# Performance work log

Measured on AMD Instinct MI355X. Metric: run time of the kernel, lower is better.

Reference implementation:

```python
import math
import jax, jax.numpy as jnp
import numpy as np

N_BASIS = 512   # number of basis signals (linear input dim)
FRAME_LEN = 64  # L, basis signal length (linear output dim)
BATCH = 8
FRAMES = 16000


def overlap_and_add(signal, frame_step):
    """Faithful jax port of the torch overlap_and_add (subframe index_add).

    signal: (..., frames, frame_length)
    returns: (..., frame_step*(frames-1)+frame_length)
    """
    *outer, frames, frame_length = signal.shape
    sub_len = math.gcd(frame_length, frame_step)
    sub_step = frame_step // sub_len
    spf = frame_length // sub_len               # subframes per frame
    output_size = frame_step * (frames - 1) + frame_length
    out_sub = output_size // sub_len

    # (..., frames*spf, sub_len)
    subframe_signal = signal.reshape(*outer, frames * spf, sub_len)

    # static scatter indices, same as torch.arange(out_sub).unfold(0, spf, sub_step)
    idx = (np.arange(frames)[:, None] * sub_step + np.arange(spf)[None, :]).reshape(-1)
    idx = jnp.asarray(idx, dtype=jnp.int32)

    result = jnp.zeros((*outer, out_sub, sub_len), dtype=signal.dtype)
    result = result.at[..., idx, :].add(subframe_signal)
    return result.reshape(*outer, out_sub * sub_len)


def setup_inputs() -> dict:
    key = jax.random.key(0)
    k1, k2 = jax.random.split(key)
    weight = jax.random.normal(k1, (BATCH, FRAMES, N_BASIS), dtype=jnp.float32)
    basis_signal_weight = jax.random.normal(k2, (FRAME_LEN, N_BASIS), dtype=jnp.float32)
    return {"weight": weight, "basis_signal_weight": basis_signal_weight}


def reference(weight, basis_signal_weight):
    L = FRAME_LEN
    # nn.Linear with bias=False: source = weight @ W.T ; W: (L, N)
    source = jnp.einsum("bkn,ln->bkl", weight, basis_signal_weight)  # (B, K, L)
    return overlap_and_add(source, L // 2)
```

## Files before the change

### kernel.cpp

```cpp
#include <hip/hip_runtime.h>
#include <hip/hip_bf16.h>

typedef __bf16 bf16x8 __attribute__((ext_vector_type(8)));
typedef __bf16 bf16x4 __attribute__((ext_vector_type(4)));
typedef float  f32x4  __attribute__((ext_vector_type(4)));

#define N_BASIS   512
#define FRAME_LEN 64
#define BATCH     8
#define FRAMES    16000
#define STEP      32
#define OUT_PER_BATCH (STEP * (FRAMES - 1) + FRAME_LEN)

#define WAVES            8
#define BLOCK            (WAVES * 64)
#define FPB              (WAVES * 16)
#define TPBATCH          (FRAMES / FPB)
#define TOTAL_TILES      (BATCH * TPBATCH)
#define TILES_PER_BLOCK  2
#define GRID             (TOTAL_TILES / TILES_PER_BLOCK)

__global__ __launch_bounds__(BLOCK, 4)
void basis_ola_kernel(const float* __restrict__ weight,
                      const float* __restrict__ basis,
                      float* __restrict__ out)
{
    __shared__ __bf16 Wlds[FRAME_LEN * N_BASIS];
    __shared__ float xbuf[2][WAVES][2][16];

    const int tid = threadIdx.x;

    for (int q = tid; q < (FRAME_LEN * N_BASIS) / 4; q += BLOCK) {
        const int e = q * 4;
        const int c = e >> 9;
        const float4 v = *(const float4*)(basis + e);
        bf16x4 b;
        b[0] = (__bf16)v.x; b[1] = (__bf16)v.y;
        b[2] = (__bf16)v.z; b[3] = (__bf16)v.w;
        *(bf16x4*)(&Wlds[e ^ ((c & 7) << 3)]) = b;
    }
    __syncthreads();

    const int wave = tid >> 6;
    const int lane = tid & 63;
    const int lo   = lane & 15;
    const int hi   = lane >> 4;

    const int g0 = blockIdx.x * TILES_PER_BLOCK;

    if (wave == 0) {
        const int bb0 = g0 / TPBATCH, t0 = g0 % TPBATCH;
        float val = 0.f;
        if (t0 > 0) {
            const int c  = 32 + (lane >> 1);
            const int kh = (lane & 1) * 256;
            const float* wr = weight + ((size_t)bb0 * FRAMES + (size_t)t0 * FPB - 1) * N_BASIS;
            for (int n = kh; n < kh + 256; n += 8) {
                const float4 a0 = *(const float4*)(wr + n);
                const float4 a1 = *(const float4*)(wr + n + 4);
                const int e = ((c << 9) + n) ^ ((c & 7) << 3);
                const bf16x8 bw = *(const bf16x8*)(&Wlds[e]);
                val += a0.x*(float)bw[0] + a0.y*(float)bw[1] + a0.z*(float)bw[2] + a0.w*(float)bw[3]
                     + a1.x*(float)bw[4] + a1.y*(float)bw[5] + a1.z*(float)bw[6] + a1.w*(float)bw[7];
            }
        }
        val += __shfl_xor(val, 1);
        if ((lane & 1) == 0) {
            const int cc = lane >> 1;
            xbuf[1][WAVES - 1][cc >> 4][cc & 15] = val;
        }
    }

    for (int ti = 0; ti < TILES_PER_BLOCK; ++ti) {
        const int g    = g0 + ti;
        const int bb   = g / TPBATCH;
        const int tile = g % TPBATCH;
        const int F0   = tile * FPB;
        const int p    = ti & 1;

        const float* arow = weight +
            ((size_t)bb * FRAMES + F0 + wave * 16 + lo) * (size_t)N_BASIS;

        f32x4 acc[4] = {};

        #pragma unroll 2
        for (int ks = 0; ks < N_BASIS / 32; ++ks) {
            const int kk = ks * 32;
            const float4 a0 = *(const float4*)(arow + kk + hi * 8);
            const float4 a1 = *(const float4*)(arow + kk + hi * 8 + 4);
            bf16x8 af;
            af[0] = (__bf16)a0.x; af[1] = (__bf16)a0.y;
            af[2] = (__bf16)a0.z; af[3] = (__bf16)a0.w;
            af[4] = (__bf16)a1.x; af[5] = (__bf16)a1.y;
            af[6] = (__bf16)a1.z; af[7] = (__bf16)a1.w;

            #pragma unroll
            for (int nt = 0; nt < 4; ++nt) {
                const int c = nt * 16 + lo;
                int e = (c << 9) + kk + hi * 8;
                e ^= (c & 7) << 3;
                const bf16x8 bfr = *(const bf16x8*)(&Wlds[e]);
                acc[nt] = __builtin_amdgcn_mfma_f32_16x16x32_bf16(af, bfr, acc[nt], 0, 0, 0);
            }
        }

        if (hi == 3) {
            xbuf[p][wave][0][lo] = acc[2][3];
            xbuf[p][wave][1][lo] = acc[3][3];
        }
        __syncthreads();

        float* ob = out + (size_t)bb * OUT_PER_BATCH;
        const int fbase = F0 + wave * 16 + hi * 4;

        #pragma unroll
        for (int nt = 0; nt < 2; ++nt) {
            const float up = __shfl_up(acc[nt + 2][3], 16);
            float pv;
            if (hi > 0)          pv = up;
            else if (wave > 0)   pv = xbuf[p][wave - 1][nt][lo];
            else if (tile > 0)   pv = xbuf[p ^ 1][WAVES - 1][nt][lo];
            else                 pv = 0.f;
            ob[32 * fbase + nt * 16 + lo] = acc[nt][0] + pv;

            #pragma unroll
            for (int r = 1; r < 4; ++r) {
                ob[32 * (fbase + r) + nt * 16 + lo] = acc[nt][r] + acc[nt + 2][r - 1];
            }
        }

        if (tile == TPBATCH - 1 && wave == WAVES - 1 && hi == 3) {
            ob[32 * FRAMES + 0 * 16 + lo] = acc[2][3];
            ob[32 * FRAMES + 1 * 16 + lo] = acc[3][3];
        }

        __syncthreads();
    }
}

extern "C" void kernel_launch(void* const* d_in, const int* in_sizes, int n_in,
                              void* d_out, int out_size, void* d_ws, size_t ws_size,
                              hipStream_t stream) {
    const float* weight = (const float*)d_in[0];
    const float* basis  = (const float*)d_in[1];
    float* out = (float*)d_out;

    basis_ola_kernel<<<GRID, BLOCK, 0, stream>>>(weight, basis, out);
}
```

Before: 55.30 us.

## Prepack basis into MFMA fragment order in workspace and drop LDS staging

A small prep kernel converts the basis to bf16 once and stores it in the exact per-lane MFMA B-fragment order in the workspace. The main kernel no longer fills a 64KB LDS tile per block; it reads fragments directly from global memory, which should hit in L2. The boundary-frame dot product now uses the fp32 basis directly. This removes per-block conversion and LDS traffic and frees LDS for occupancy. The cost is an extra kernel launch and B operands fetched from cache instead of LDS inside the inner loop.

```diff
diff --git a/kernel.cpp b/kernel.cpp
--- a/kernel.cpp
+++ b/kernel.cpp
@@ -20,27 +20,32 @@
 #define TILES_PER_BLOCK  2
 #define GRID             (TOTAL_TILES / TILES_PER_BLOCK)
 
+__global__ __launch_bounds__(256)
+void prep_basis(const float* __restrict__ basis, __bf16* __restrict__ wsb) {
+    const int t  = blockIdx.x * blockDim.x + threadIdx.x;
+    const int fr = t >> 6;
+    const int l  = t & 63;
+    const int c  = (fr & 3) * 16 + (l & 15);
+    const int n  = (fr >> 2) * 32 + (l >> 4) * 8;
+    const float4 a0 = *(const float4*)(basis + c * N_BASIS + n);
+    const float4 a1 = *(const float4*)(basis + c * N_BASIS + n + 4);
+    bf16x8 b;
+    b[0] = (__bf16)a0.x; b[1] = (__bf16)a0.y;
+    b[2] = (__bf16)a0.z; b[3] = (__bf16)a0.w;
+    b[4] = (__bf16)a1.x; b[5] = (__bf16)a1.y;
+    b[6] = (__bf16)a1.z; b[7] = (__bf16)a1.w;
+    *(bf16x8*)(wsb + (size_t)t * 8) = b;
+}
+
 __global__ __launch_bounds__(BLOCK, 4)
 void basis_ola_kernel(const float* __restrict__ weight,
                       const float* __restrict__ basis,
+                      const __bf16* __restrict__ wsb,
                       float* __restrict__ out)
 {
-    __shared__ __bf16 Wlds[FRAME_LEN * N_BASIS];
     __shared__ float xbuf[2][WAVES][2][16];
 
-    const int tid = threadIdx.x;
-
-    for (int q = tid; q < (FRAME_LEN * N_BASIS) / 4; q += BLOCK) {
-        const int e = q * 4;
-        const int c = e >> 9;
-        const float4 v = *(const float4*)(basis + e);
-        bf16x4 b;
-        b[0] = (__bf16)v.x; b[1] = (__bf16)v.y;
-        b[2] = (__bf16)v.z; b[3] = (__bf16)v.w;
-        *(bf16x4*)(&Wlds[e ^ ((c & 7) << 3)]) = b;
-    }
-    __syncthreads();
-
+    const int tid  = threadIdx.x;
     const int wave = tid >> 6;
     const int lane = tid & 63;
     const int lo   = lane & 15;
@@ -55,13 +60,11 @@
             const int c  = 32 + (lane >> 1);
             const int kh = (lane & 1) * 256;
             const float* wr = weight + ((size_t)bb0 * FRAMES + (size_t)t0 * FPB - 1) * N_BASIS;
-            for (int n = kh; n < kh + 256; n += 8) {
-                const float4 a0 = *(const float4*)(wr + n);
-                const float4 a1 = *(const float4*)(wr + n + 4);
-                const int e = ((c << 9) + n) ^ ((c & 7) << 3);
-                const bf16x8 bw = *(const bf16x8*)(&Wlds[e]);
-                val += a0.x*(float)bw[0] + a0.y*(float)bw[1] + a0.z*(float)bw[2] + a0.w*(float)bw[3]
-                     + a1.x*(float)bw[4] + a1.y*(float)bw[5] + a1.z*(float)bw[6] + a1.w*(float)bw[7];
+            const float* br = basis + (size_t)c * N_BASIS;
+            for (int n = kh; n < kh + 256; n += 4) {
+                const float4 a = *(const float4*)(wr + n);
+                const float4 w = *(const float4*)(br + n);
+                val += a.x * w.x + a.y * w.y + a.z * w.z + a.w * w.w;
             }
         }
         val += __shfl_xor(val, 1);
@@ -94,12 +97,10 @@
             af[4] = (__bf16)a1.x; af[5] = (__bf16)a1.y;
             af[6] = (__bf16)a1.z; af[7] = (__bf16)a1.w;
 
+            const __bf16* fb = wsb + (size_t)(ks * 4) * 512 + lane * 8;
             #pragma unroll
             for (int nt = 0; nt < 4; ++nt) {
-                const int c = nt * 16 + lo;
-                int e = (c << 9) + kk + hi * 8;
-                e ^= (c & 7) << 3;
-                const bf16x8 bfr = *(const bf16x8*)(&Wlds[e]);
+                const bf16x8 bfr = *(const bf16x8*)(fb + nt * 512);
                 acc[nt] = __builtin_amdgcn_mfma_f32_16x16x32_bf16(af, bfr, acc[nt], 0, 0, 0);
             }
         }
@@ -144,6 +145,8 @@
     const float* weight = (const float*)d_in[0];
     const float* basis  = (const float*)d_in[1];
     float* out = (float*)d_out;
+    __bf16* wsb = (__bf16*)d_ws;
 
-    basis_ola_kernel<<<GRID, BLOCK, 0, stream>>>(weight, basis, out);
+    prep_basis<<<16, 256, 0, stream>>>(basis, wsb);
+    basis_ola_kernel<<<GRID, BLOCK, 0, stream>>>(weight, basis, wsb, out);
 }
```

New measurement: 75.70 us. +36.9%, slower.

## Prefetch activation tiles early, use nontemporal loads/stores, and overlap basis staging

Applied to the files above, without the earlier changes.

Issues the first two k-steps of activation loads for tile 0 before staging the basis into LDS, and prefetches tile 1's first loads before tile 0's epilogue. The activation and output streams use nontemporal loads and stores to reduce cache pollution. The boundary-frame dot product now reads fp32 basis from global memory instead of LDS, so it can run without waiting for a barrier. The basis staging is widened to 8 elements per thread. The aim is to hide global-load latency behind the basis setup and the epilogue. The boundary term now uses fp32 basis where it used bf16 before, which slightly changes its rounding.

```diff
diff --git a/kernel.cpp b/kernel.cpp
--- a/kernel.cpp
+++ b/kernel.cpp
@@ -2,7 +2,6 @@
 #include <hip/hip_bf16.h>
 
 typedef __bf16 bf16x8 __attribute__((ext_vector_type(8)));
-typedef __bf16 bf16x4 __attribute__((ext_vector_type(4)));
 typedef float  f32x4  __attribute__((ext_vector_type(4)));
 
 #define N_BASIS   512
@@ -20,48 +19,129 @@
 #define TILES_PER_BLOCK  2
 #define GRID             (TOTAL_TILES / TILES_PER_BLOCK)
 
+__device__ __forceinline__ f32x4 ldnt(const float* p) {
+    return __builtin_nontemporal_load((const f32x4*)p);
+}
+
+__device__ __forceinline__ void kstep(const f32x4 a0, const f32x4 a1,
+                                      const __bf16* W, int kk, int lo, int hi,
+                                      f32x4 acc[4]) {
+    bf16x8 af;
+    af[0] = (__bf16)a0[0]; af[1] = (__bf16)a0[1];
+    af[2] = (__bf16)a0[2]; af[3] = (__bf16)a0[3];
+    af[4] = (__bf16)a1[0]; af[5] = (__bf16)a1[1];
+    af[6] = (__bf16)a1[2]; af[7] = (__bf16)a1[3];
+    #pragma unroll
+    for (int nt = 0; nt < 4; ++nt) {
+        const int c = nt * 16 + lo;
+        int e = (c << 9) + kk + hi * 8;
+        e ^= (c & 7) << 3;
+        const bf16x8 b = *(const bf16x8*)(&W[e]);
+        acc[nt] = __builtin_amdgcn_mfma_f32_16x16x32_bf16(af, b, acc[nt], 0, 0, 0);
+    }
+}
+
+__device__ __forceinline__ void tile_compute(const float* __restrict__ arow,
+                                             const __bf16* W,
+                                             const f32x4 q0, const f32x4 q1,
+                                             const f32x4 q2, const f32x4 q3,
+                                             int lo, int hi, f32x4 acc[4]) {
+    kstep(q0, q1, W, 0,  lo, hi, acc);
+    kstep(q2, q3, W, 32, lo, hi, acc);
+    #pragma unroll 2
+    for (int ks = 2; ks < 16; ++ks) {
+        const int kk = ks * 32;
+        const f32x4 a0 = ldnt(arow + kk + hi * 8);
+        const f32x4 a1 = ldnt(arow + kk + hi * 8 + 4);
+        kstep(a0, a1, W, kk, lo, hi, acc);
+    }
+}
+
+__device__ __forceinline__ void epilogue(const f32x4 acc[4],
+                                         float* __restrict__ out,
+                                         float (&xbuf)[2][WAVES][2][16],
+                                         int P, int tile, int bb, int F0,
+                                         int wave, int lo, int hi) {
+    if (hi == 3) {
+        xbuf[P][wave][0][lo] = acc[2][3];
+        xbuf[P][wave][1][lo] = acc[3][3];
+    }
+    __syncthreads();
+
+    float* ob = out + (size_t)bb * OUT_PER_BATCH;
+    const int fbase = F0 + wave * 16 + hi * 4;
+
+    #pragma unroll
+    for (int nt = 0; nt < 2; ++nt) {
+        const float up = __shfl_up(acc[nt + 2][3], 16);
+        float pv;
+        if (hi > 0)          pv = up;
+        else if (wave > 0)   pv = xbuf[P][wave - 1][nt][lo];
+        else if (tile > 0)   pv = xbuf[P ^ 1][WAVES - 1][nt][lo];
+        else                 pv = 0.f;
+        __builtin_nontemporal_store(acc[nt][0] + pv, &ob[32 * fbase + nt * 16 + lo]);
+        #pragma unroll
+        for (int r = 1; r < 4; ++r)
+            __builtin_nontemporal_store(acc[nt][r] + acc[nt + 2][r - 1],
+                                        &ob[32 * (fbase + r) + nt * 16 + lo]);
+    }
+
+    if (tile == TPBATCH - 1 && wave == WAVES - 1 && hi == 3) {
+        __builtin_nontemporal_store(acc[2][3], &ob[32 * FRAMES + lo]);
+        __builtin_nontemporal_store(acc[3][3], &ob[32 * FRAMES + 16 + lo]);
+    }
+}
+
 __global__ __launch_bounds__(BLOCK, 4)
 void basis_ola_kernel(const float* __restrict__ weight,
                       const float* __restrict__ basis,
                       float* __restrict__ out)
 {
     __shared__ __bf16 Wlds[FRAME_LEN * N_BASIS];
-    __shared__ float xbuf[2][WAVES][2][16];
+    __shared__ float  xbuf[2][WAVES][2][16];
 
-    const int tid = threadIdx.x;
-
-    for (int q = tid; q < (FRAME_LEN * N_BASIS) / 4; q += BLOCK) {
-        const int e = q * 4;
-        const int c = e >> 9;
-        const float4 v = *(const float4*)(basis + e);
-        bf16x4 b;
-        b[0] = (__bf16)v.x; b[1] = (__bf16)v.y;
-        b[2] = (__bf16)v.z; b[3] = (__bf16)v.w;
-        *(bf16x4*)(&Wlds[e ^ ((c & 7) << 3)]) = b;
-    }
-    __syncthreads();
-
+    const int tid  = threadIdx.x;
     const int wave = tid >> 6;
     const int lane = tid & 63;
     const int lo   = lane & 15;
     const int hi   = lane >> 4;
 
-    const int g0 = blockIdx.x * TILES_PER_BLOCK;
+    const int g0  = blockIdx.x * TILES_PER_BLOCK;
+    const int bb0 = g0 / TPBATCH, t0 = g0 % TPBATCH;
+    const int g1  = g0 + 1;
+    const int bb1 = g1 / TPBATCH, t1 = g1 % TPBATCH;
+
+    const float* arow0 = weight + ((size_t)bb0 * FRAMES + t0 * FPB + wave * 16 + lo) * N_BASIS;
+    f32x4 q0 = ldnt(arow0 + hi * 8);
+    f32x4 q1 = ldnt(arow0 + hi * 8 + 4);
+    f32x4 q2 = ldnt(arow0 + 32 + hi * 8);
+    f32x4 q3 = ldnt(arow0 + 32 + hi * 8 + 4);
+
+    for (int q = tid; q < (FRAME_LEN * N_BASIS) / 8; q += BLOCK) {
+        const int e = q * 8;
+        const int c = e >> 9;
+        const f32x4 v0 = *(const f32x4*)(basis + e);
+        const f32x4 v1 = *(const f32x4*)(basis + e + 4);
+        bf16x8 b;
+        b[0] = (__bf16)v0[0]; b[1] = (__bf16)v0[1];
+        b[2] = (__bf16)v0[2]; b[3] = (__bf16)v0[3];
+        b[4] = (__bf16)v1[0]; b[5] = (__bf16)v1[1];
+        b[6] = (__bf16)v1[2]; b[7] = (__bf16)v1[3];
+        *(bf16x8*)(&Wlds[e ^ ((c & 7) << 3)]) = b;
+    }
 
     if (wave == 0) {
-        const int bb0 = g0 / TPBATCH, t0 = g0 % TPBATCH;
         float val = 0.f;
         if (t0 > 0) {
             const int c  = 32 + (lane >> 1);
             const int kh = (lane & 1) * 256;
             const float* wr = weight + ((size_t)bb0 * FRAMES + (size_t)t0 * FPB - 1) * N_BASIS;
-            for (int n = kh; n < kh + 256; n += 8) {
-                const float4 a0 = *(const float4*)(wr + n);
-                const float4 a1 = *(const float4*)(wr + n + 4);
-                const int e = ((c << 9) + n) ^ ((c & 7) << 3);
-                const bf16x8 bw = *(const bf16x8*)(&Wlds[e]);
-                val += a0.x*(float)bw[0] + a0.y*(float)bw[1] + a0.z*(float)bw[2] + a0.w*(float)bw[3]
-                     + a1.x*(float)bw[4] + a1.y*(float)bw[5] + a1.z*(float)bw[6] + a1.w*(float)bw[7];
+            const float* br = basis + (size_t)c * N_BASIS;
+            #pragma unroll 4
+            for (int n = kh; n < kh + 256; n += 4) {
+                const f32x4 a = *(const f32x4*)(wr + n);
+                const f32x4 w = *(const f32x4*)(br + n);
+                val += a[0]*w[0] + a[1]*w[1] + a[2]*w[2] + a[3]*w[3];
             }
         }
         val += __shfl_xor(val, 1);
@@ -70,72 +150,23 @@
             xbuf[1][WAVES - 1][cc >> 4][cc & 15] = val;
         }
     }
+    __syncthreads();
 
-    for (int ti = 0; ti < TILES_PER_BLOCK; ++ti) {
-        const int g    = g0 + ti;
-        const int bb   = g / TPBATCH;
-        const int tile = g % TPBATCH;
-        const int F0   = tile * FPB;
-        const int p    = ti & 1;
+    f32x4 acc0[4] = {};
+    tile_compute(arow0, Wlds, q0, q1, q2, q3, lo, hi, acc0);
 
-        const float* arow = weight +
-            ((size_t)bb * FRAMES + F0 + wave * 16 + lo) * (size_t)N_BASIS;
+    const float* arow1 = weight + ((size_t)bb1 * FRAMES + t1 * FPB + wave * 16 + lo) * N_BASIS;
+    q0 = ldnt(arow1 + hi * 8);
+    q1 = ldnt(arow1 + hi * 8 + 4);
+    q2 = ldnt(arow1 + 32 + hi * 8);
+    q3 = ldnt(arow1 + 32 + hi * 8 + 4);
 
-        f32x4 acc[4] = {};
+    epilogue(acc0, out, xbuf, 0, t0, bb0, t0 * FPB, wave, lo, hi);
+    __syncthreads();
 
-        #pragma unroll 2
-        for (int ks = 0; ks < N_BASIS / 32; ++ks) {
-            const int kk = ks * 32;
-            const float4 a0 = *(const float4*)(arow + kk + hi * 8);
-            const float4 a1 = *(const float4*)(arow + kk + hi * 8 + 4);
-            bf16x8 af;
-            af[0] = (__bf16)a0.x; af[1] = (__bf16)a0.y;
-            af[2] = (__bf16)a0.z; af[3] = (__bf16)a0.w;
-            af[4] = (__bf16)a1.x; af[5] = (__bf16)a1.y;
-            af[6] = (__bf16)a1.z; af[7] = (__bf16)a1.w;
-
-            #pragma unroll
-            for (int nt = 0; nt < 4; ++nt) {
-                const int c = nt * 16 + lo;
-                int e = (c << 9) + kk + hi * 8;
-                e ^= (c & 7) << 3;
-                const bf16x8 bfr = *(const bf16x8*)(&Wlds[e]);
-                acc[nt] = __builtin_amdgcn_mfma_f32_16x16x32_bf16(af, bfr, acc[nt], 0, 0, 0);
-            }
-        }
-
-        if (hi == 3) {
-            xbuf[p][wave][0][lo] = acc[2][3];
-            xbuf[p][wave][1][lo] = acc[3][3];
-        }
-        __syncthreads();
-
-        float* ob = out + (size_t)bb * OUT_PER_BATCH;
-        const int fbase = F0 + wave * 16 + hi * 4;
-
-        #pragma unroll
-        for (int nt = 0; nt < 2; ++nt) {
-            const float up = __shfl_up(acc[nt + 2][3], 16);
-            float pv;
-            if (hi > 0)          pv = up;
-            else if (wave > 0)   pv = xbuf[p][wave - 1][nt][lo];
-            else if (tile > 0)   pv = xbuf[p ^ 1][WAVES - 1][nt][lo];
-            else                 pv = 0.f;
-            ob[32 * fbase + nt * 16 + lo] = acc[nt][0] + pv;
-
-            #pragma unroll
-            for (int r = 1; r < 4; ++r) {
-                ob[32 * (fbase + r) + nt * 16 + lo] = acc[nt][r] + acc[nt + 2][r - 1];
-            }
-        }
-
-        if (tile == TPBATCH - 1 && wave == WAVES - 1 && hi == 3) {
-            ob[32 * FRAMES + 0 * 16 + lo] = acc[2][3];
-            ob[32 * FRAMES + 1 * 16 + lo] = acc[3][3];
-        }
-
-        __syncthreads();
-    }
+    f32x4 acc1[4] = {};
+    tile_compute(arow1, Wlds, q0, q1, q2, q3, lo, hi, acc1);
+    epilogue(acc1, out, xbuf, 1, t1, bb1, t1 * FPB, wave, lo, hi);
 }
 
 extern "C" void kernel_launch(void* const* d_in, const int* in_sizes, int n_in,
```

After: 65.57 us. 18.6% more time.
